# Kernel tuning notes

Hardware: AMD Instinct MI355X
Metric: run time of the kernel (lower is better)

Reference implementation:

```python
import jax, jax.numpy as jnp
from jax import lax
import numpy as np

T, B, I, H, OUT = 1024, 32, 128, 512, 10


def _lstm_layer(x, W_ih, W_hh, b):
    """PyTorch-convention LSTM layer. x: [T,B,in], W_ih: [4H,in], W_hh: [4H,H], b: [4H].
    Gate order: i, f, g, o. Returns all hidden states [T,B,H]."""
    hdim = W_hh.shape[1]
    # Precompute input projections for all timesteps (big GEMM, compute-bound).
    x_proj = jnp.einsum('tbi,gi->tbg', x, W_ih) + b  # [T,B,4H]

    def step(carry, xp_t):
        h, c = carry
        gates = xp_t + h @ W_hh.T  # [B,4H]
        i_g, f_g, g_g, o_g = jnp.split(gates, 4, axis=-1)
        i_g = jax.nn.sigmoid(i_g)
        f_g = jax.nn.sigmoid(f_g)
        g_g = jnp.tanh(g_g)
        o_g = jax.nn.sigmoid(o_g)
        c = f_g * c + i_g * g_g
        h = o_g * jnp.tanh(c)
        return (h, c), h

    h0 = jnp.zeros((x.shape[1], hdim), x.dtype)
    c0 = jnp.zeros((x.shape[1], hdim), x.dtype)
    _, hs = lax.scan(step, (h0, c0), x_proj)
    return hs  # [T,B,H]


def setup_inputs() -> dict:
    key = jax.random.key(0)
    ks = jax.random.split(key, 9)
    s1 = 1.0 / np.sqrt(H)  # PyTorch LSTM init scale U(-1/sqrt(H), 1/sqrt(H)); use scaled normal
    return {
        'data': jax.random.normal(ks[0], (T, B, I), jnp.float32),
        'W_ih1': jax.random.normal(ks[1], (4 * H, I), jnp.float32) * s1,
        'W_hh1': jax.random.normal(ks[2], (4 * H, H), jnp.float32) * s1,
        'b1': jax.random.normal(ks[3], (4 * H,), jnp.float32) * s1,
        'W_ih2': jax.random.normal(ks[4], (4 * H, H), jnp.float32) * s1,
        'W_hh2': jax.random.normal(ks[5], (4 * H, H), jnp.float32) * s1,
        'b2': jax.random.normal(ks[6], (4 * H,), jnp.float32) * s1,
        'W3': jax.random.normal(ks[7], (OUT, H), jnp.float32) * s1,
        'b3': jax.random.normal(ks[8], (OUT,), jnp.float32) * s1,
    }


def reference(data, W_ih1, W_hh1, b1, W_ih2, W_hh2, b2, W3, b3):
    h = _lstm_layer(data, W_ih1, W_hh1, b1)   # [T,B,H]
    h = _lstm_layer(h, W_ih2, W_hh2, b2)      # [T,B,H]
    logits = jnp.einsum('tbh,oh->tbo', h, W3) + b3  # [T,B,OUT]
    return jax.nn.softmax(logits, axis=2)
```

## Files before the change

### kernel.cpp

```cpp
#include <hip/hip_runtime.h>
#include <cstdint>
#include <cstddef>

#define TCHUNK 128
#define NCHUNK 8
#define BATCH 32
#define IDIM 128
#define HDIM 512
#define GDIM 2048
#define ODIM 10
#define NBLK 256
#define XPSTEP (GDIM * BATCH)

typedef float f4 __attribute__((ext_vector_type(4)));

__device__ __forceinline__ void llc_load4x2(const float* p0, const float* p1,
                                            f4& a, f4& b) {
  asm volatile("global_load_dwordx4 %0, %2, off sc0 sc1\n\t"
               "global_load_dwordx4 %1, %3, off sc0 sc1\n\t"
               "s_waitcnt vmcnt(0)"
               : "=&v"(a), "=&v"(b) : "v"(p0), "v"(p1) : "memory");
}
__device__ __forceinline__ void llc_store(float* p, float v) {
  asm volatile("global_store_dword %0, %1, off sc0 sc1" :: "v"(p), "v"(v) : "memory");
}
__device__ __forceinline__ void llc_store_u32(unsigned* p, unsigned v) {
  asm volatile("global_store_dword %0, %1, off sc0 sc1" :: "v"(p), "v"(v) : "memory");
}
__device__ __forceinline__ unsigned llc_load_u32(const unsigned* p) {
  unsigned v;
  asm volatile("global_load_dword %0, %1, off sc0 sc1\n\ts_waitcnt vmcnt(0)"
               : "=v"(v) : "v"(p) : "memory");
  return v;
}

__device__ __forceinline__ float quad_sum(float x) {
  int t = __builtin_amdgcn_update_dpp(0, __float_as_int(x), 0xB1, 0xF, 0xF, true);
  x += __int_as_float(t);
  t = __builtin_amdgcn_update_dpp(0, __float_as_int(x), 0x4E, 0xF, 0xF, true);
  x += __int_as_float(t);
  return x;
}

template<int K>
__launch_bounds__(256, 2)
__global__ void proj_kernel(const float* __restrict__ X,
                            const float* __restrict__ W,
                            const float* __restrict__ bias,
                            float* __restrict__ P) {
  __shared__ float Xs[8][132];
  __shared__ float Ws[8][132];
  const int tid = threadIdx.x;
  const int n0 = blockIdx.x * 128;
  const int m0 = blockIdx.y * 128;
  const int tx = tid & 15, ty = tid >> 4;
  const int lm = tid >> 1;
  const int kq = (tid & 1) * 4;
  float acc[8][8];
#pragma unroll
  for (int i = 0; i < 8; ++i)
#pragma unroll
    for (int j = 0; j < 8; ++j) acc[i][j] = 0.f;

  for (int k0 = 0; k0 < K; k0 += 8) {
    const float4 xv = *(const float4*)&X[(size_t)(m0 + lm) * K + k0 + kq];
    const float4 wv = *(const float4*)&W[(size_t)(n0 + lm) * K + k0 + kq];
    __syncthreads();
    Xs[kq + 0][lm] = xv.x; Xs[kq + 1][lm] = xv.y; Xs[kq + 2][lm] = xv.z; Xs[kq + 3][lm] = xv.w;
    Ws[kq + 0][lm] = wv.x; Ws[kq + 1][lm] = wv.y; Ws[kq + 2][lm] = wv.z; Ws[kq + 3][lm] = wv.w;
    __syncthreads();
#pragma unroll
    for (int kk = 0; kk < 8; ++kk) {
      float a[8], b[8];
      *(float4*)&a[0] = *(const float4*)&Xs[kk][ty * 8];
      *(float4*)&a[4] = *(const float4*)&Xs[kk][ty * 8 + 4];
      *(float4*)&b[0] = *(const float4*)&Ws[kk][tx * 8];
      *(float4*)&b[4] = *(const float4*)&Ws[kk][tx * 8 + 4];
#pragma unroll
      for (int i = 0; i < 8; ++i)
#pragma unroll
        for (int j = 0; j < 8; ++j) acc[i][j] += a[i] * b[j];
    }
  }
  const int mb = m0 + ty * 8;
  const int t  = mb >> 5;
  const int b0 = mb & 31;
#pragma unroll
  for (int j = 0; j < 8; ++j) {
    const int n = n0 + tx * 8 + j;
    const float bj = bias[n];
    float* dst = &P[((size_t)t * GDIM + n) * BATCH + b0];
#pragma unroll
    for (int i = 0; i < 8; ++i) dst[i] = acc[i][j] + bj;
  }
}

__launch_bounds__(256, 1)
__global__ void scan_kernel(const float* __restrict__ xp,
                            const float* __restrict__ Whh,
                            float* __restrict__ hout,
                            float* __restrict__ hx,
                            float* __restrict__ ccur,
                            unsigned* __restrict__ flg,
                            int phase0, int first) {
  __shared__ float h_s[2048];
  __shared__ float red[1024];
  __shared__ float gate_s[256];
  __shared__ float lds_pad[22528];

  const int tid = threadIdx.x;
  const int bid = blockIdx.x;
  const int g = bid & 7, rank = bid >> 3;
  const int w = tid >> 6, l = tid & 63;
  const int rq = l >> 2, s4 = l & 3;

  float* hxg = hx + g * 4096;
  unsigned* flgg = flg + g * 64;

  const int kbase = 128 * w + 32 * s4;
  const int m = (4 * w + s4) & 15;
  const int hbase = 4 * kbase;
  float wreg[4][32];
#pragma unroll
  for (int r = 0; r < 4; ++r) {
    const int rl = 4 * rq + r;
    const int grow = (rl >> 4) * HDIM + rank * 16 + (rl & 15);
    const float* wp = &Whh[(size_t)grow * HDIM + kbase];
#pragma unroll
    for (int q8 = 0; q8 < 8; ++q8) {
      const f4 wv = *(const f4*)&wp[q8 * 4];
      wreg[r][q8 * 4 + 0] = wv.x; wreg[r][q8 * 4 + 1] = wv.y;
      wreg[r][q8 * 4 + 2] = wv.z; wreg[r][q8 * 4 + 3] = wv.w;
    }
  }

  const int rl_c = tid >> 2, b_c = tid & 3;
  const size_t xpoff = (size_t)((tid >> 6) * HDIM + rank * 16 + (rl_c & 15)) * BATCH
                       + g * 4 + b_c;
  const int jj = l >> 2, bb = l & 3;

  float c_st = 0.f;
  if (!first && w == 0) c_st = ccur[(size_t)(g * 4 + bb) * HDIM + rank * 16 + jj];

  auto stage_h = [&](int pp) {
    const float* hp = hxg + pp * 2048;
    f4 a, b;
    llc_load4x2(hp + 8 * tid, hp + 8 * tid + 4, a, b);
    const int mm = (tid >> 4) & 15;
    *(f4*)&h_s[4 * ((2 * tid) ^ mm)] = a;
    *(f4*)&h_s[4 * ((2 * tid + 1) ^ mm)] = b;
  };

  stage_h(0);
  __syncthreads();

  for (int tt = 0; tt < TCHUNK; ++tt) {
    const float xpv = xp[(size_t)tt * XPSTEP + xpoff];

    float acc[4][4];
#pragma unroll
    for (int r = 0; r < 4; ++r)
#pragma unroll
      for (int b = 0; b < 4; ++b) acc[r][b] = 0.f;
#pragma unroll
    for (int idx = 0; idx < 32; ++idx) {
      const f4 hv = *(const f4*)&h_s[hbase + 4 * (idx ^ m)];
#pragma unroll
      for (int r = 0; r < 4; ++r) {
        acc[r][0] += wreg[r][idx] * hv.x;
        acc[r][1] += wreg[r][idx] * hv.y;
        acc[r][2] += wreg[r][idx] * hv.z;
        acc[r][3] += wreg[r][idx] * hv.w;
      }
    }
#pragma unroll
    for (int r = 0; r < 4; ++r)
#pragma unroll
      for (int b = 0; b < 4; ++b) acc[r][b] = quad_sum(acc[r][b]);
    f4 outv;
#pragma unroll
    for (int b = 0; b < 4; ++b) {
      const float v01 = (s4 & 1) ? acc[1][b] : acc[0][b];
      const float v23 = (s4 & 1) ? acc[3][b] : acc[2][b];
      outv[b] = (s4 & 2) ? v23 : v01;
    }
    *(f4*)&red[w * 256 + 4 * l] = outv;
    __syncthreads();

    const float pre = red[tid] + red[256 + tid] + red[512 + tid] + red[768 + tid] + xpv;
    gate_s[tid] = (w == 2) ? tanhf(pre) : 1.f / (1.f + __expf(-pre));
    __syncthreads();

    const int wp_ = (tt + 1) & 1;
    const unsigned ph = (unsigned)(phase0 + tt + 1);
    if (w == 0) {
      const float ig = gate_s[l];
      const float fg = gate_s[64 + l];
      const float gg = gate_s[128 + l];
      const float og = gate_s[192 + l];
      c_st = fg * c_st + ig * gg;
      const float hval = og * tanhf(c_st);
      const int slot = rank * 16 + jj;
      llc_store(hxg + wp_ * 2048 + 4 * slot + bb, hval);
      hout[(size_t)tt * (BATCH * HDIM) + (size_t)(g * 4 + bb) * HDIM + slot] = hval;
      asm volatile("s_waitcnt vmcnt(0)" ::: "memory");
      if (tid == 0) llc_store_u32(flgg + rank, ph);
      const unsigned* fp = flgg + (l & 31);
      while (true) {
        const unsigned fv = llc_load_u32(fp);
        if (__all((int)(fv >= ph))) break;
        __builtin_amdgcn_s_sleep(2);
      }
    }
    __syncthreads();
    stage_h(wp_);
    __syncthreads();
  }
  if (w == 0) ccur[(size_t)(g * 4 + bb) * HDIM + rank * 16 + jj] = c_st;
  if (__float_as_uint(c_st) == 0xDEADBEEFu) lds_pad[tid] = c_st;
}

__launch_bounds__(256, 2)
__global__ void head_kernel(const float* __restrict__ h2,
                            const float* __restrict__ W3,
                            const float* __restrict__ b3,
                            float* __restrict__ outp) {
  const int tid = threadIdx.x;
  const int lane = tid & 63;
  const int wv = tid >> 6;
  const int row = blockIdx.x * 4 + wv;
  const float* hrow = &h2[(size_t)row * HDIM];
  float hreg[8];
  *(float4*)&hreg[0] = *(const float4*)&hrow[lane * 8];
  *(float4*)&hreg[4] = *(const float4*)&hrow[lane * 8 + 4];
  float logit[ODIM];
#pragma unroll
  for (int o = 0; o < ODIM; ++o) {
    const float* wrow = &W3[o * HDIM + lane * 8];
    float w[8];
    *(float4*)&w[0] = *(const float4*)&wrow[0];
    *(float4*)&w[4] = *(const float4*)&wrow[4];
    float pp = 0.f;
#pragma unroll
    for (int j = 0; j < 8; ++j) pp += hreg[j] * w[j];
#pragma unroll
    for (int off = 32; off > 0; off >>= 1) pp += __shfl_xor(pp, off);
    logit[o] = pp + b3[o];
  }
  float mx = logit[0];
#pragma unroll
  for (int o = 1; o < ODIM; ++o) mx = fmaxf(mx, logit[o]);
  float ssum = 0.f;
#pragma unroll
  for (int o = 0; o < ODIM; ++o) { logit[o] = __expf(logit[o] - mx); ssum += logit[o]; }
  const float inv = 1.f / ssum;
  if (lane == 0) {
    float* dst = &outp[(size_t)row * ODIM];
#pragma unroll
    for (int o = 0; o < ODIM; ++o) dst[o] = logit[o] * inv;
  }
}

extern "C" void kernel_launch(void* const* d_in, const int* in_sizes, int n_in,
                              void* d_out, int out_size, void* d_ws, size_t ws_size,
                              hipStream_t stream) {
  const float* data  = (const float*)d_in[0];
  const float* W_ih1 = (const float*)d_in[1];
  const float* W_hh1 = (const float*)d_in[2];
  const float* b1    = (const float*)d_in[3];
  const float* W_ih2 = (const float*)d_in[4];
  const float* W_hh2 = (const float*)d_in[5];
  const float* b2    = (const float*)d_in[6];
  const float* W3    = (const float*)d_in[7];
  const float* b3    = (const float*)d_in[8];
  float* outp = (float*)d_out;

  char* ws = (char*)d_ws;
  size_t off = 0;
  float* xp    = (float*)(ws + off); off += (size_t)TCHUNK * GDIM * BATCH * 4;
  float* h1c   = (float*)(ws + off); off += (size_t)TCHUNK * BATCH * HDIM * 4;
  float* h2c   = (float*)(ws + off); off += (size_t)TCHUNK * BATCH * HDIM * 4;
  float* hx1   = (float*)(ws + off); off += 8 * 2 * 2048 * 4;
  float* hx2   = (float*)(ws + off); off += 8 * 2 * 2048 * 4;
  float* ccur1 = (float*)(ws + off); off += BATCH * HDIM * 4;
  float* ccur2 = (float*)(ws + off); off += BATCH * HDIM * 4;
  unsigned* flg1 = (unsigned*)(ws + off); off += 8 * 64 * 4;
  unsigned* flg2 = (unsigned*)(ws + off); off += 8 * 64 * 4;
  if (off > ws_size) return;

  hipMemsetAsync(hx1, 0, 8 * 2 * 2048 * 4, stream);
  hipMemsetAsync(hx2, 0, 8 * 2 * 2048 * 4, stream);
  hipMemsetAsync(flg1, 0, 8 * 64 * 4, stream);
  hipMemsetAsync(flg2, 0, 8 * 64 * 4, stream);

  const dim3 pgrid(GDIM / 128, (TCHUNK * BATCH) / 128);
  for (int c = 0; c < NCHUNK; ++c) {
    const float* xin = data + (size_t)c * TCHUNK * BATCH * IDIM;
    proj_kernel<IDIM><<<pgrid, 256, 0, stream>>>(xin, W_ih1, b1, xp);
    scan_kernel<<<NBLK, 256, 0, stream>>>(xp, W_hh1, h1c, hx1, ccur1, flg1,
                                          c * TCHUNK, c == 0);
    proj_kernel<HDIM><<<pgrid, 256, 0, stream>>>(h1c, W_ih2, b2, xp);
    scan_kernel<<<NBLK, 256, 0, stream>>>(xp, W_hh2, h2c, hx2, ccur2, flg2,
                                          c * TCHUNK, c == 0);
    head_kernel<<<(TCHUNK * BATCH) / 4, 256, 0, stream>>>(
        h2c, W3, b3, outp + (size_t)c * TCHUNK * BATCH * ODIM);
  }
}
```

Measured before the change: 10.23 ms.

## Pipeline LSTM scan per batch column with staggered per-wave flags and async LDS staging

Restructures the recurrent scan so each block handles its four batch columns as four substeps. Each wave owns one column's gate math, and the grid-wide flag signalling and polling are split per column. Staging of the next hidden state uses global_load_lds directly into LDS and overlaps with compute on the other columns. This is meant to hide cross-block sync latency behind useful work instead of serialising all columns behind one flag barrier per step. It adds more barriers per timestep, more complex flag bookkeeping, and a bounded spin guard that could silently proceed on timeout.

```diff
diff --git a/kernel.cpp b/kernel.cpp
--- a/kernel.cpp
+++ b/kernel.cpp
@@ -14,13 +14,6 @@
 
 typedef float f4 __attribute__((ext_vector_type(4)));
 
-__device__ __forceinline__ void llc_load4x2(const float* p0, const float* p1,
-                                            f4& a, f4& b) {
-  asm volatile("global_load_dwordx4 %0, %2, off sc0 sc1\n\t"
-               "global_load_dwordx4 %1, %3, off sc0 sc1\n\t"
-               "s_waitcnt vmcnt(0)"
-               : "=&v"(a), "=&v"(b) : "v"(p0), "v"(p1) : "memory");
-}
 __device__ __forceinline__ void llc_store(float* p, float v) {
   asm volatile("global_store_dword %0, %1, off sc0 sc1" :: "v"(p), "v"(v) : "memory");
 }
@@ -33,7 +26,6 @@
                : "=v"(v) : "v"(p) : "memory");
   return v;
 }
-
 __device__ __forceinline__ float quad_sum(float x) {
   int t = __builtin_amdgcn_update_dpp(0, __float_as_int(x), 0xB1, 0xF, 0xF, true);
   x += __int_as_float(t);
@@ -95,6 +87,101 @@
   }
 }
 
+#define BARRIER() do {                                                      \
+    asm volatile("s_waitcnt lgkmcnt(0)" ::: "memory");                      \
+    __builtin_amdgcn_sched_barrier(0);                                      \
+    __builtin_amdgcn_s_barrier();                                           \
+    __builtin_amdgcn_sched_barrier(0);                                      \
+  } while (0)
+
+#define STAGE_ISSUE(CH, TPP)                                                \
+  {                                                                         \
+    const float* slice_ = hxg + ((CH) * 2 + ((TPP) & 1)) * 512;             \
+    _Pragma("unroll")                                                       \
+    for (int i_ = 0; i_ < 8; ++i_) {                                        \
+      __builtin_amdgcn_global_load_lds(                                     \
+          (const __attribute__((address_space(1))) unsigned*)(slice_ + karr[i_]), \
+          (__attribute__((address_space(3))) unsigned*)&h_s[(CH)][64 * i_], \
+          4, 0, 17 );                                            \
+    }                                                                       \
+  }
+
+#define POLL_SPIN(CH, TGT, FV)                                              \
+  {                                                                         \
+    int guard_ = 0;                                                         \
+    while (!__all((int)((FV) >= (unsigned)(TGT))) && ++guard_ < 3000000) {  \
+      __builtin_amdgcn_s_sleep(1);                                          \
+      (FV) = llc_load_u32(flgg + (CH) * 32 + (l & 31));                     \
+    }                                                                       \
+  }
+
+#define SUBSTEP(C)                                                          \
+  {                                                                         \
+    constexpr int c_ = (C);                                                 \
+    constexpr int fwv = (c_ + 3) & 3, swv = (c_ + 2) & 3, dwv = (c_ + 1) & 3; \
+    const int tpp = t + (c_ >= 2 ? 1 : 0);                                  \
+    const bool dostage = (tpp < TCHUNK);                                    \
+    unsigned fv0 = 0xFFFFFFFFu;                                             \
+    if (w == fwv) {                        \
+      asm volatile("s_waitcnt vmcnt(0)" ::: "memory");                      \
+      if (l == 0)                                                           \
+        llc_store_u32(flgg + fwv * 32 + rank,                               \
+                      (unsigned)(base + t + (c_ >= 1 ? 1 : 0)));            \
+    }                                                                       \
+    if (w == swv && dostage) {                   \
+      asm volatile("global_load_dword %0, %1, off sc0 sc1"                  \
+                   : "=v"(fv0) : "v"(flgg + swv * 32 + (l & 31)) : "memory"); \
+    }                                                                       \
+                   \
+    {                                                                       \
+      float a0 = 0.f, a1 = 0.f, a2 = 0.f, a3 = 0.f;                         \
+      const float* hb = &h_s[c_][kb];                                       \
+      _Pragma("unroll")                                                     \
+      for (int i4 = 0; i4 < 8; ++i4) {                                      \
+        const f4 hv = *(const f4*)&hb[4 * (i4 ^ (2 * s4))];                 \
+        a0 += wreg[0][i4*4+0]*hv.x + wreg[0][i4*4+1]*hv.y                   \
+            + wreg[0][i4*4+2]*hv.z + wreg[0][i4*4+3]*hv.w;                  \
+        a1 += wreg[1][i4*4+0]*hv.x + wreg[1][i4*4+1]*hv.y                   \
+            + wreg[1][i4*4+2]*hv.z + wreg[1][i4*4+3]*hv.w;                  \
+        a2 += wreg[2][i4*4+0]*hv.x + wreg[2][i4*4+1]*hv.y                   \
+            + wreg[2][i4*4+2]*hv.z + wreg[2][i4*4+3]*hv.w;                  \
+        a3 += wreg[3][i4*4+0]*hv.x + wreg[3][i4*4+1]*hv.y                   \
+            + wreg[3][i4*4+2]*hv.z + wreg[3][i4*4+3]*hv.w;                  \
+      }                                                                     \
+      a0 = quad_sum(a0); a1 = quad_sum(a1);                                 \
+      a2 = quad_sum(a2); a3 = quad_sum(a3);                                 \
+      const float v01 = (s4 & 1) ? a1 : a0;                                 \
+      const float v23 = (s4 & 1) ? a3 : a2;                                 \
+      red[w][l] = (s4 & 2) ? v23 : v01;                                     \
+    }                                                                       \
+    BARRIER();                                                              \
+    if (w == c_) {                            \
+      float pre = red[0][l] + red[1][l] + red[2][l] + red[3][l] + xpv;      \
+      const float act = ((l >> 4) == 2) ? tanhf(pre)                        \
+                                        : 1.f / (1.f + __expf(-pre));       \
+      const int j = l & 15;                                                 \
+      const float ig = __shfl(act, j),      fg = __shfl(act, 16 + j);       \
+      const float gg = __shfl(act, 32 + j), og = __shfl(act, 48 + j);       \
+      if (l < 16) {                                                         \
+        c_st = fg * c_st + ig * gg;                                         \
+        const float hval = og * tanhf(c_st);                                \
+        llc_store(hxg + (c_ * 2 + ((t + 1) & 1)) * 512 + slot16 + l, hval); \
+        hout[(size_t)t * (BATCH * HDIM) + (size_t)(g * 4 + c_) * HDIM       \
+             + slot16 + l] = hval;                                          \
+      }                                                                     \
+    }                                                                       \
+    if (w == swv && dostage) {               \
+      asm volatile("s_waitcnt vmcnt(0)" ::: "memory");                      \
+      POLL_SPIN(swv, base + tpp, fv0);                                      \
+      STAGE_ISSUE(swv, tpp);                                                \
+      xpv = xp[(size_t)tpp * XPSTEP + xprow];                               \
+    }                                                                       \
+    if (w == dwv) {                           \
+      asm volatile("s_waitcnt vmcnt(0)" ::: "memory");                      \
+    }                                                                       \
+    BARRIER();                                                              \
+  }
+
 __launch_bounds__(256, 1)
 __global__ void scan_kernel(const float* __restrict__ xp,
                             const float* __restrict__ Whh,
@@ -102,122 +189,69 @@
                             float* __restrict__ hx,
                             float* __restrict__ ccur,
                             unsigned* __restrict__ flg,
-                            int phase0, int first) {
-  __shared__ float h_s[2048];
-  __shared__ float red[1024];
-  __shared__ float gate_s[256];
-  __shared__ float lds_pad[22528];
-
-  const int tid = threadIdx.x;
-  const int bid = blockIdx.x;
+                            int base, int first) {
+  __shared__ float h_s[4][512];
+  __shared__ float red[4][64];
+  __shared__ float pad[19456];
+
+  const int tid = threadIdx.x, bid = blockIdx.x;
   const int g = bid & 7, rank = bid >> 3;
   const int w = tid >> 6, l = tid & 63;
-  const int rq = l >> 2, s4 = l & 3;
+  const int s4 = l & 3, rq = l >> 2;
 
   float* hxg = hx + g * 4096;
-  unsigned* flgg = flg + g * 64;
-
-  const int kbase = 128 * w + 32 * s4;
-  const int m = (4 * w + s4) & 15;
-  const int hbase = 4 * kbase;
+  unsigned* flgg = flg + g * 128;
+
   float wreg[4][32];
+  const int kb = 128 * w + 32 * s4;
 #pragma unroll
   for (int r = 0; r < 4; ++r) {
     const int rl = 4 * rq + r;
-    const int grow = (rl >> 4) * HDIM + rank * 16 + (rl & 15);
-    const float* wp = &Whh[(size_t)grow * HDIM + kbase];
+    const float* wp = &Whh[(size_t)((rl >> 4) * HDIM + rank * 16 + (rl & 15)) * HDIM + kb];
 #pragma unroll
     for (int q8 = 0; q8 < 8; ++q8) {
-      const f4 wv = *(const f4*)&wp[q8 * 4];
-      wreg[r][q8 * 4 + 0] = wv.x; wreg[r][q8 * 4 + 1] = wv.y;
-      wreg[r][q8 * 4 + 2] = wv.z; wreg[r][q8 * 4 + 3] = wv.w;
+      const f4 v = *(const f4*)&wp[q8 * 4];
+      wreg[r][q8 * 4 + 0] = v.x; wreg[r][q8 * 4 + 1] = v.y;
+      wreg[r][q8 * 4 + 2] = v.z; wreg[r][q8 * 4 + 3] = v.w;
     }
   }
 
-  const int rl_c = tid >> 2, b_c = tid & 3;
-  const size_t xpoff = (size_t)((tid >> 6) * HDIM + rank * 16 + (rl_c & 15)) * BATCH
-                       + g * 4 + b_c;
-  const int jj = l >> 2, bb = l & 3;
-
+  int karr[8];
+#pragma unroll
+  for (int i = 0; i < 8; ++i) {
+    const int L = 64 * i + l;
+    karr[i] = L ^ (((L >> 5) & 3) << 3);
+  }
+
+  const int slot16 = rank * 16;
+  const size_t xprow = (size_t)((l >> 4) * HDIM + slot16 + (l & 15)) * BATCH + g * 4 + w;
   float c_st = 0.f;
-  if (!first && w == 0) c_st = ccur[(size_t)(g * 4 + bb) * HDIM + rank * 16 + jj];
-
-  auto stage_h = [&](int pp) {
-    const float* hp = hxg + pp * 2048;
-    f4 a, b;
-    llc_load4x2(hp + 8 * tid, hp + 8 * tid + 4, a, b);
-    const int mm = (tid >> 4) & 15;
-    *(f4*)&h_s[4 * ((2 * tid) ^ mm)] = a;
-    *(f4*)&h_s[4 * ((2 * tid + 1) ^ mm)] = b;
-  };
-
-  stage_h(0);
-  __syncthreads();
-
-  for (int tt = 0; tt < TCHUNK; ++tt) {
-    const float xpv = xp[(size_t)tt * XPSTEP + xpoff];
-
-    float acc[4][4];
-#pragma unroll
-    for (int r = 0; r < 4; ++r)
-#pragma unroll
-      for (int b = 0; b < 4; ++b) acc[r][b] = 0.f;
-#pragma unroll
-    for (int idx = 0; idx < 32; ++idx) {
-      const f4 hv = *(const f4*)&h_s[hbase + 4 * (idx ^ m)];
-#pragma unroll
-      for (int r = 0; r < 4; ++r) {
-        acc[r][0] += wreg[r][idx] * hv.x;
-        acc[r][1] += wreg[r][idx] * hv.y;
-        acc[r][2] += wreg[r][idx] * hv.z;
-        acc[r][3] += wreg[r][idx] * hv.w;
-      }
-    }
-#pragma unroll
-    for (int r = 0; r < 4; ++r)
-#pragma unroll
-      for (int b = 0; b < 4; ++b) acc[r][b] = quad_sum(acc[r][b]);
-    f4 outv;
-#pragma unroll
-    for (int b = 0; b < 4; ++b) {
-      const float v01 = (s4 & 1) ? acc[1][b] : acc[0][b];
-      const float v23 = (s4 & 1) ? acc[3][b] : acc[2][b];
-      outv[b] = (s4 & 2) ? v23 : v01;
-    }
-    *(f4*)&red[w * 256 + 4 * l] = outv;
-    __syncthreads();
-
-    const float pre = red[tid] + red[256 + tid] + red[512 + tid] + red[768 + tid] + xpv;
-    gate_s[tid] = (w == 2) ? tanhf(pre) : 1.f / (1.f + __expf(-pre));
-    __syncthreads();
-
-    const int wp_ = (tt + 1) & 1;
-    const unsigned ph = (unsigned)(phase0 + tt + 1);
-    if (w == 0) {
-      const float ig = gate_s[l];
-      const float fg = gate_s[64 + l];
-      const float gg = gate_s[128 + l];
-      const float og = gate_s[192 + l];
-      c_st = fg * c_st + ig * gg;
-      const float hval = og * tanhf(c_st);
-      const int slot = rank * 16 + jj;
-      llc_store(hxg + wp_ * 2048 + 4 * slot + bb, hval);
-      hout[(size_t)tt * (BATCH * HDIM) + (size_t)(g * 4 + bb) * HDIM + slot] = hval;
-      asm volatile("s_waitcnt vmcnt(0)" ::: "memory");
-      if (tid == 0) llc_store_u32(flgg + rank, ph);
-      const unsigned* fp = flgg + (l & 31);
-      while (true) {
-        const unsigned fv = llc_load_u32(fp);
-        if (__all((int)(fv >= ph))) break;
-        __builtin_amdgcn_s_sleep(2);
-      }
-    }
-    __syncthreads();
-    stage_h(wp_);
-    __syncthreads();
-  }
-  if (w == 0) ccur[(size_t)(g * 4 + bb) * HDIM + rank * 16 + jj] = c_st;
-  if (__float_as_uint(c_st) == 0xDEADBEEFu) lds_pad[tid] = c_st;
+  if (!first && l < 16) c_st = ccur[(size_t)(g * 4 + w) * HDIM + slot16 + l];
+  float xpv = 0.f;
+
+  if (w < 2) {
+    unsigned fv = llc_load_u32(flgg + w * 32 + (l & 31));
+    POLL_SPIN(w, base, fv);
+    STAGE_ISSUE(w, 0);
+    xpv = xp[xprow];
+    asm volatile("s_waitcnt vmcnt(0)" ::: "memory");
+  }
+  BARRIER();
+
+#pragma unroll 1
+  for (int t = 0; t < TCHUNK; ++t) {
+    SUBSTEP(0)
+    SUBSTEP(1)
+    SUBSTEP(2)
+    SUBSTEP(3)
+  }
+
+  if (w == 3) {
+    asm volatile("s_waitcnt vmcnt(0)" ::: "memory");
+    if (l == 0) llc_store_u32(flgg + 3 * 32 + rank, (unsigned)(base + TCHUNK));
+  }
+  if (l < 16) ccur[(size_t)(g * 4 + w) * HDIM + slot16 + l] = c_st;
+  ((volatile float*)pad)[tid] = c_st;
 }
 
 __launch_bounds__(256, 2)
@@ -280,18 +314,18 @@
   float* xp    = (float*)(ws + off); off += (size_t)TCHUNK * GDIM * BATCH * 4;
   float* h1c   = (float*)(ws + off); off += (size_t)TCHUNK * BATCH * HDIM * 4;
   float* h2c   = (float*)(ws + off); off += (size_t)TCHUNK * BATCH * HDIM * 4;
-  float* hx1   = (float*)(ws + off); off += 8 * 2 * 2048 * 4;
-  float* hx2   = (float*)(ws + off); off += 8 * 2 * 2048 * 4;
+  float* hx1   = (float*)(ws + off); off += 8 * 4 * 2 * 512 * 4;
+  float* hx2   = (float*)(ws + off); off += 8 * 4 * 2 * 512 * 4;
   float* ccur1 = (float*)(ws + off); off += BATCH * HDIM * 4;
   float* ccur2 = (float*)(ws + off); off += BATCH * HDIM * 4;
-  unsigned* flg1 = (unsigned*)(ws + off); off += 8 * 64 * 4;
-  unsigned* flg2 = (unsigned*)(ws + off); off += 8 * 64 * 4;
+  unsigned* flg1 = (unsigned*)(ws + off); off += 8 * 4 * 32 * 4;
+  unsigned* flg2 = (unsigned*)(ws + off); off += 8 * 4 * 32 * 4;
   if (off > ws_size) return;
 
-  hipMemsetAsync(hx1, 0, 8 * 2 * 2048 * 4, stream);
-  hipMemsetAsync(hx2, 0, 8 * 2 * 2048 * 4, stream);
-  hipMemsetAsync(flg1, 0, 8 * 64 * 4, stream);
-  hipMemsetAsync(flg2, 0, 8 * 64 * 4, stream);
+  hipMemsetAsync(hx1, 0, 8 * 4 * 2 * 512 * 4, stream);
+  hipMemsetAsync(hx2, 0, 8 * 4 * 2 * 512 * 4, stream);
+  hipMemsetAsync(flg1, 0, 8 * 4 * 32 * 4, stream);
+  hipMemsetAsync(flg2, 0, 8 * 4 * 32 * 4, stream);
 
   const dim3 pgrid(GDIM / 128, (TCHUNK * BATCH) / 128);
   for (int c = 0; c < NCHUNK; ++c) {
```

Result: faster. 9.394 ms (-8.1%).

## Replace flag-based grid barrier with sentinel-polled per-timestep hidden-state slabs

Applied to the files above, without the earlier changes.

The scan kernel no longer uses a per-step flag counter and spin barrier. Each timestep's hidden state now goes into its own slab, pre-filled with a 0xFF sentinel, and consumers poll the slab data directly until no sentinel remains. This removes the extra flag store/load round trip and the block-wide barrier after the exchange, letting producers run ahead. It also switches the inner loops to packed float2 FMAs and uses lightweight s_barrier macros. The cost is a large memset per chunk plus a carry-over memcpy, and correctness now depends on NaN-pattern sentinels never matching real values; a guard timeout could silently read stale data.

```diff
diff --git a/kernel.cpp b/kernel.cpp
--- a/kernel.cpp
+++ b/kernel.cpp
@@ -11,29 +11,15 @@
 #define ODIM 10
 #define NBLK 256
 #define XPSTEP (GDIM * BATCH)
+#define SLAB_F 16384
+#define SLAB_B (SLAB_F * 4)
 
 typedef float f4 __attribute__((ext_vector_type(4)));
-
-__device__ __forceinline__ void llc_load4x2(const float* p0, const float* p1,
-                                            f4& a, f4& b) {
-  asm volatile("global_load_dwordx4 %0, %2, off sc0 sc1\n\t"
-               "global_load_dwordx4 %1, %3, off sc0 sc1\n\t"
-               "s_waitcnt vmcnt(0)"
-               : "=&v"(a), "=&v"(b) : "v"(p0), "v"(p1) : "memory");
-}
+typedef float f2 __attribute__((ext_vector_type(2)));
+
 __device__ __forceinline__ void llc_store(float* p, float v) {
   asm volatile("global_store_dword %0, %1, off sc0 sc1" :: "v"(p), "v"(v) : "memory");
 }
-__device__ __forceinline__ void llc_store_u32(unsigned* p, unsigned v) {
-  asm volatile("global_store_dword %0, %1, off sc0 sc1" :: "v"(p), "v"(v) : "memory");
-}
-__device__ __forceinline__ unsigned llc_load_u32(const unsigned* p) {
-  unsigned v;
-  asm volatile("global_load_dword %0, %1, off sc0 sc1\n\ts_waitcnt vmcnt(0)"
-               : "=v"(v) : "v"(p) : "memory");
-  return v;
-}
-
 __device__ __forceinline__ float quad_sum(float x) {
   int t = __builtin_amdgcn_update_dpp(0, __float_as_int(x), 0xB1, 0xF, 0xF, true);
   x += __int_as_float(t);
@@ -41,6 +27,13 @@
   x += __int_as_float(t);
   return x;
 }
+
+#define BARRIER() do {                                                      \
+    asm volatile("s_waitcnt lgkmcnt(0)" ::: "memory");                      \
+    __builtin_amdgcn_sched_barrier(0);                                      \
+    __builtin_amdgcn_s_barrier();                                           \
+    __builtin_amdgcn_sched_barrier(0);                                      \
+  } while (0)
 
 template<int K>
 __launch_bounds__(256, 2)
@@ -56,11 +49,11 @@
   const int tx = tid & 15, ty = tid >> 4;
   const int lm = tid >> 1;
   const int kq = (tid & 1) * 4;
-  float acc[8][8];
+  f2 acc2[8][4];
 #pragma unroll
   for (int i = 0; i < 8; ++i)
 #pragma unroll
-    for (int j = 0; j < 8; ++j) acc[i][j] = 0.f;
+    for (int j = 0; j < 4; ++j) acc2[i][j] = (f2){0.f, 0.f};
 
   for (int k0 = 0; k0 < K; k0 += 8) {
     const float4 xv = *(const float4*)&X[(size_t)(m0 + lm) * K + k0 + kq];
@@ -71,15 +64,16 @@
     __syncthreads();
 #pragma unroll
     for (int kk = 0; kk < 8; ++kk) {
-      float a[8], b[8];
+      float a[8];
       *(float4*)&a[0] = *(const float4*)&Xs[kk][ty * 8];
       *(float4*)&a[4] = *(const float4*)&Xs[kk][ty * 8 + 4];
-      *(float4*)&b[0] = *(const float4*)&Ws[kk][tx * 8];
-      *(float4*)&b[4] = *(const float4*)&Ws[kk][tx * 8 + 4];
+      f2 b2[4];
+#pragma unroll
+      for (int jp = 0; jp < 4; ++jp) b2[jp] = *(const f2*)&Ws[kk][tx * 8 + 2 * jp];
 #pragma unroll
       for (int i = 0; i < 8; ++i)
 #pragma unroll
-        for (int j = 0; j < 8; ++j) acc[i][j] += a[i] * b[j];
+        for (int jp = 0; jp < 4; ++jp) acc2[i][jp] += b2[jp] * a[i];
     }
   }
   const int mb = m0 + ty * 8;
@@ -91,7 +85,8 @@
     const float bj = bias[n];
     float* dst = &P[((size_t)t * GDIM + n) * BATCH + b0];
 #pragma unroll
-    for (int i = 0; i < 8; ++i) dst[i] = acc[i][j] + bj;
+    for (int i = 0; i < 8; ++i)
+      dst[i] = ((j & 1) ? acc2[i][j >> 1].y : acc2[i][j >> 1].x) + bj;
   }
 }
 
@@ -99,125 +94,119 @@
 __global__ void scan_kernel(const float* __restrict__ xp,
                             const float* __restrict__ Whh,
                             float* __restrict__ hout,
-                            float* __restrict__ hx,
+                            float* __restrict__ hb,
                             float* __restrict__ ccur,
-                            unsigned* __restrict__ flg,
-                            int phase0, int first) {
+                            int first) {
   __shared__ float h_s[2048];
   __shared__ float red[1024];
   __shared__ float gate_s[256];
-  __shared__ float lds_pad[22528];
-
-  const int tid = threadIdx.x;
-  const int bid = blockIdx.x;
-  const int g = bid & 7, rank = bid >> 3;
+  __shared__ float pad[17408];
+
+  const int tid = threadIdx.x, bid = blockIdx.x;
+  const int g = bid & 7, rank = bid >> 3, slot16 = rank * 16;
   const int w = tid >> 6, l = tid & 63;
-  const int rq = l >> 2, s4 = l & 3;
-
-  float* hxg = hx + g * 4096;
-  unsigned* flgg = flg + g * 64;
-
-  const int kbase = 128 * w + 32 * s4;
-  const int m = (4 * w + s4) & 15;
-  const int hbase = 4 * kbase;
+  const int s4 = l & 3, rq = l >> 2;
+  const int sg = 4 * w + s4;
+  const int cx = sg & 7;
+  const int kb = 32 * sg;
+
   float wreg[4][32];
 #pragma unroll
   for (int r = 0; r < 4; ++r) {
     const int rl = 4 * rq + r;
-    const int grow = (rl >> 4) * HDIM + rank * 16 + (rl & 15);
-    const float* wp = &Whh[(size_t)grow * HDIM + kbase];
-#pragma unroll
-    for (int q8 = 0; q8 < 8; ++q8) {
-      const f4 wv = *(const f4*)&wp[q8 * 4];
-      wreg[r][q8 * 4 + 0] = wv.x; wreg[r][q8 * 4 + 1] = wv.y;
-      wreg[r][q8 * 4 + 2] = wv.z; wreg[r][q8 * 4 + 3] = wv.w;
-    }
-  }
-
-  const int rl_c = tid >> 2, b_c = tid & 3;
-  const size_t xpoff = (size_t)((tid >> 6) * HDIM + rank * 16 + (rl_c & 15)) * BATCH
-                       + g * 4 + b_c;
+    const float* wp = Whh + (size_t)((rl >> 4) * HDIM + slot16 + (rl & 15)) * HDIM + kb;
+#pragma unroll
+    for (int e = 0; e < 32; ++e) wreg[r][e] = wp[e ^ cx];
+  }
+
+  const int cl = l >> 4, m = l & 15;
+  const int sig = (4 * w + (m >> 2)) & 7;
+  int dsaddr[8];
+#pragma unroll
+  for (int i = 0; i < 8; ++i)
+    dsaddr[i] = 4 * (128 * w + 8 * m + (i ^ sig)) + cl;
+  const int srcoff = cl * 512 + 128 * w + 8 * m;
+
+  const int qg = tid >> 6, jg = (tid >> 2) & 15, bg = tid & 3;
+  const float* xq = xp + (size_t)(qg * HDIM + slot16 + jg) * BATCH + g * 4 + bg;
+
   const int jj = l >> 2, bb = l & 3;
 
   float c_st = 0.f;
-  if (!first && w == 0) c_st = ccur[(size_t)(g * 4 + bb) * HDIM + rank * 16 + jj];
-
-  auto stage_h = [&](int pp) {
-    const float* hp = hxg + pp * 2048;
-    f4 a, b;
-    llc_load4x2(hp + 8 * tid, hp + 8 * tid + 4, a, b);
-    const int mm = (tid >> 4) & 15;
-    *(f4*)&h_s[4 * ((2 * tid) ^ mm)] = a;
-    *(f4*)&h_s[4 * ((2 * tid + 1) ^ mm)] = b;
-  };
-
-  stage_h(0);
-  __syncthreads();
-
+  if (!first && w == 0) c_st = ccur[(size_t)(g * 4 + bb) * HDIM + slot16 + jj];
+
+  const float* hptr = &h_s[128 * sg];
+
+#pragma unroll 1
   for (int tt = 0; tt < TCHUNK; ++tt) {
-    const float xpv = xp[(size_t)tt * XPSTEP + xpoff];
-
-    float acc[4][4];
-#pragma unroll
-    for (int r = 0; r < 4; ++r)
-#pragma unroll
-      for (int b = 0; b < 4; ++b) acc[r][b] = 0.f;
-#pragma unroll
-    for (int idx = 0; idx < 32; ++idx) {
-      const f4 hv = *(const f4*)&h_s[hbase + 4 * (idx ^ m)];
+    const float* src = hb + (size_t)tt * SLAB_F + g * 2048 + srcoff;
+    f4 va, vb;
+    int guard = 0;
+    while (true) {
+      asm volatile("global_load_dwordx4 %0, %2, off sc0 sc1\n\t"
+                   "global_load_dwordx4 %1, %3, off sc0 sc1\n\t"
+                   "s_waitcnt vmcnt(0)"
+                   : "=&v"(va), "=&v"(vb) : "v"(src), "v"(src + 4) : "memory");
+      const bool ok =
+          __float_as_uint(va.x) != 0xFFFFFFFFu && __float_as_uint(va.y) != 0xFFFFFFFFu &&
+          __float_as_uint(va.z) != 0xFFFFFFFFu && __float_as_uint(va.w) != 0xFFFFFFFFu &&
+          __float_as_uint(vb.x) != 0xFFFFFFFFu && __float_as_uint(vb.y) != 0xFFFFFFFFu &&
+          __float_as_uint(vb.z) != 0xFFFFFFFFu && __float_as_uint(vb.w) != 0xFFFFFFFFu;
+      if (__all(ok) || ++guard > 100000) break;
+      __builtin_amdgcn_s_sleep(2);
+    }
+    h_s[dsaddr[0]] = va.x; h_s[dsaddr[1]] = va.y;
+    h_s[dsaddr[2]] = va.z; h_s[dsaddr[3]] = va.w;
+    h_s[dsaddr[4]] = vb.x; h_s[dsaddr[5]] = vb.y;
+    h_s[dsaddr[6]] = vb.z; h_s[dsaddr[7]] = vb.w;
+    const float xpv = xq[(size_t)tt * XPSTEP];
+    BARRIER();
+
+    f2 a01[4], a23[4];
+#pragma unroll
+    for (int r = 0; r < 4; ++r) { a01[r] = (f2){0.f, 0.f}; a23[r] = (f2){0.f, 0.f}; }
+#pragma unroll
+    for (int kk = 0; kk < 32; ++kk) {
+      const f4 hv = *(const f4*)&hptr[4 * kk];
+      const f2 h01 = {hv.x, hv.y}, h23 = {hv.z, hv.w};
 #pragma unroll
       for (int r = 0; r < 4; ++r) {
-        acc[r][0] += wreg[r][idx] * hv.x;
-        acc[r][1] += wreg[r][idx] * hv.y;
-        acc[r][2] += wreg[r][idx] * hv.z;
-        acc[r][3] += wreg[r][idx] * hv.w;
+        a01[r] += h01 * wreg[r][kk];
+        a23[r] += h23 * wreg[r][kk];
       }
     }
 #pragma unroll
-    for (int r = 0; r < 4; ++r)
-#pragma unroll
-      for (int b = 0; b < 4; ++b) acc[r][b] = quad_sum(acc[r][b]);
-    f4 outv;
-#pragma unroll
-    for (int b = 0; b < 4; ++b) {
-      const float v01 = (s4 & 1) ? acc[1][b] : acc[0][b];
-      const float v23 = (s4 & 1) ? acc[3][b] : acc[2][b];
-      outv[b] = (s4 & 2) ? v23 : v01;
-    }
-    *(f4*)&red[w * 256 + 4 * l] = outv;
-    __syncthreads();
+    for (int r = 0; r < 4; ++r) {
+      a01[r].x = quad_sum(a01[r].x); a01[r].y = quad_sum(a01[r].y);
+      a23[r].x = quad_sum(a23[r].x); a23[r].y = quad_sum(a23[r].y);
+    }
+    f2 r01, r23;
+    { const f2 v0 = (s4 & 1) ? a01[1] : a01[0];
+      const f2 v1 = (s4 & 1) ? a01[3] : a01[2];
+      r01 = (s4 & 2) ? v1 : v0;
+      const f2 u0 = (s4 & 1) ? a23[1] : a23[0];
+      const f2 u1 = (s4 & 1) ? a23[3] : a23[2];
+      r23 = (s4 & 2) ? u1 : u0; }
+    *(f4*)&red[(w << 8) + 4 * l] = (f4){r01.x, r01.y, r23.x, r23.y};
+    BARRIER();
 
     const float pre = red[tid] + red[256 + tid] + red[512 + tid] + red[768 + tid] + xpv;
-    gate_s[tid] = (w == 2) ? tanhf(pre) : 1.f / (1.f + __expf(-pre));
-    __syncthreads();
-
-    const int wp_ = (tt + 1) & 1;
-    const unsigned ph = (unsigned)(phase0 + tt + 1);
+    gate_s[tid] = (qg == 2) ? tanhf(pre) : 1.f / (1.f + __expf(-pre));
+    BARRIER();
+
     if (w == 0) {
-      const float ig = gate_s[l];
-      const float fg = gate_s[64 + l];
-      const float gg = gate_s[128 + l];
-      const float og = gate_s[192 + l];
+      const float ig = gate_s[jj * 4 + bb];
+      const float fg = gate_s[64 + jj * 4 + bb];
+      const float gg = gate_s[128 + jj * 4 + bb];
+      const float og = gate_s[192 + jj * 4 + bb];
       c_st = fg * c_st + ig * gg;
       const float hval = og * tanhf(c_st);
-      const int slot = rank * 16 + jj;
-      llc_store(hxg + wp_ * 2048 + 4 * slot + bb, hval);
-      hout[(size_t)tt * (BATCH * HDIM) + (size_t)(g * 4 + bb) * HDIM + slot] = hval;
-      asm volatile("s_waitcnt vmcnt(0)" ::: "memory");
-      if (tid == 0) llc_store_u32(flgg + rank, ph);
-      const unsigned* fp = flgg + (l & 31);
-      while (true) {
-        const unsigned fv = llc_load_u32(fp);
-        if (__all((int)(fv >= ph))) break;
-        __builtin_amdgcn_s_sleep(2);
-      }
-    }
-    __syncthreads();
-    stage_h(wp_);
-    __syncthreads();
-  }
-  if (w == 0) ccur[(size_t)(g * 4 + bb) * HDIM + rank * 16 + jj] = c_st;
-  if (__float_as_uint(c_st) == 0xDEADBEEFu) lds_pad[tid] = c_st;
+      llc_store(hb + (size_t)(tt + 1) * SLAB_F + g * 2048 + bb * 512 + slot16 + jj, hval);
+      hout[(size_t)tt * (BATCH * HDIM) + (size_t)(g * 4 + bb) * HDIM + slot16 + jj] = hval;
+    }
+  }
+  if (w == 0) ccur[(size_t)(g * 4 + bb) * HDIM + slot16 + jj] = c_st;
+  ((volatile float*)pad)[tid] = c_st;
 }
 
 __launch_bounds__(256, 2)
@@ -280,28 +269,34 @@
   float* xp    = (float*)(ws + off); off += (size_t)TCHUNK * GDIM * BATCH * 4;
   float* h1c   = (float*)(ws + off); off += (size_t)TCHUNK * BATCH * HDIM * 4;
   float* h2c   = (float*)(ws + off); off += (size_t)TCHUNK * BATCH * HDIM * 4;
-  float* hx1   = (float*)(ws + off); off += 8 * 2 * 2048 * 4;
-  float* hx2   = (float*)(ws + off); off += 8 * 2 * 2048 * 4;
+  float* hb1   = (float*)(ws + off); off += (size_t)(TCHUNK + 1) * SLAB_B;
+  float* hb2   = (float*)(ws + off); off += (size_t)(TCHUNK + 1) * SLAB_B;
   float* ccur1 = (float*)(ws + off); off += BATCH * HDIM * 4;
   float* ccur2 = (float*)(ws + off); off += BATCH * HDIM * 4;
-  unsigned* flg1 = (unsigned*)(ws + off); off += 8 * 64 * 4;
-  unsigned* flg2 = (unsigned*)(ws + off); off += 8 * 64 * 4;
   if (off > ws_size) return;
 
-  hipMemsetAsync(hx1, 0, 8 * 2 * 2048 * 4, stream);
-  hipMemsetAsync(hx2, 0, 8 * 2 * 2048 * 4, stream);
-  hipMemsetAsync(flg1, 0, 8 * 64 * 4, stream);
-  hipMemsetAsync(flg2, 0, 8 * 64 * 4, stream);
+  hipMemsetAsync(hb1, 0x00, SLAB_B, stream);
+  hipMemsetAsync((char*)hb1 + SLAB_B, 0xFF, (size_t)TCHUNK * SLAB_B, stream);
+  hipMemsetAsync(hb2, 0x00, SLAB_B, stream);
+  hipMemsetAsync((char*)hb2 + SLAB_B, 0xFF, (size_t)TCHUNK * SLAB_B, stream);
 
   const dim3 pgrid(GDIM / 128, (TCHUNK * BATCH) / 128);
   for (int c = 0; c < NCHUNK; ++c) {
     const float* xin = data + (size_t)c * TCHUNK * BATCH * IDIM;
     proj_kernel<IDIM><<<pgrid, 256, 0, stream>>>(xin, W_ih1, b1, xp);
-    scan_kernel<<<NBLK, 256, 0, stream>>>(xp, W_hh1, h1c, hx1, ccur1, flg1,
-                                          c * TCHUNK, c == 0);
+    scan_kernel<<<NBLK, 256, 0, stream>>>(xp, W_hh1, h1c, hb1, ccur1, c == 0);
+    if (c < NCHUNK - 1) {
+      hipMemcpyAsync(hb1, (char*)hb1 + (size_t)TCHUNK * SLAB_B, SLAB_B,
+                     hipMemcpyDeviceToDevice, stream);
+      hipMemsetAsync((char*)hb1 + SLAB_B, 0xFF, (size_t)TCHUNK * SLAB_B, stream);
+    }
     proj_kernel<HDIM><<<pgrid, 256, 0, stream>>>(h1c, W_ih2, b2, xp);
-    scan_kernel<<<NBLK, 256, 0, stream>>>(xp, W_hh2, h2c, hx2, ccur2, flg2,
-                                          c * TCHUNK, c == 0);
+    scan_kernel<<<NBLK, 256, 0, stream>>>(xp, W_hh2, h2c, hb2, ccur2, c == 0);
+    if (c < NCHUNK - 1) {
+      hipMemcpyAsync(hb2, (char*)hb2 + (size_t)TCHUNK * SLAB_B, SLAB_B,
+                     hipMemcpyDeviceToDevice, stream);
+      hipMemsetAsync((char*)hb2 + SLAB_B, 0xFF, (size_t)TCHUNK * SLAB_B, stream);
+    }
     head_kernel<<<(TCHUNK * BATCH) / 4, 256, 0, stream>>>(
         h2c, W3, b3, outp + (size_t)c * TCHUNK * BATCH * ODIM);
   }
```

Measured after the change: 8.822 ms. 1.16x faster.
